# Kernel tuning notes

Measured on AMD Instinct MI355X. Metric: run time of the kernel, lower is better.

Reference implementation:

```python
import jax, jax.numpy as jnp
import numpy as np

DT = 0.05
DELAY = int(1.0 / DT)  # 20 steps of synaptic delay
NUM_ASCS = 2
R_MEM = 0.1     # membrane resistance
SIGMA_V = 1.0   # sigmoid smoothing of spiking nonlinearity
V_RESET = 0.0

B, T, IN, HID, OUT = 64, 200, 512, 1024, 512


def setup_inputs() -> dict:
    key = jax.random.key(0)
    ks = jax.random.split(key, 10)
    return {
        "x": jax.random.normal(ks[0], (B, T, IN), dtype=jnp.float32),
        "W_in": jax.random.normal(ks[1], (IN, HID), dtype=jnp.float32) / np.sqrt(IN),
        "W_lat": jax.random.normal(ks[2], (HID, HID), dtype=jnp.float32) / np.sqrt(HID),
        "thresh": jax.random.normal(ks[3], (1, HID), dtype=jnp.float32) * 0.1,
        "trans_k_m": jax.random.normal(ks[4], (1, HID), dtype=jnp.float32) * 0.1,
        "trans_asc_k": jax.random.normal(ks[5], (NUM_ASCS, 1, HID), dtype=jnp.float32) * 0.1,
        "asc_amp": jax.random.normal(ks[6], (NUM_ASCS, 1, HID), dtype=jnp.float32) * 0.1,
        "trans_asc_r": jax.random.normal(ks[7], (NUM_ASCS, 1, HID), dtype=jnp.float32) * 0.1,
        "W_out": jax.random.normal(ks[8], (OUT, HID), dtype=jnp.float32) / np.sqrt(HID),
        "b_out": jax.random.normal(ks[9], (OUT,), dtype=jnp.float32) * 0.01,
    }


def _glifr_rnn(x, W_in, W_lat, thresh, trans_k_m, trans_asc_k, asc_amp, trans_asc_r, W_out, b_out):
    Bx, Tx, _ = x.shape
    H = W_lat.shape[0]
    # rate transforms keep dt*k in (0,1); r in (-1,1)
    k_m = jax.nn.sigmoid(trans_k_m) / DT          # [1,H]
    k_asc = jax.nn.sigmoid(trans_asc_k) / DT      # [A,1,H]
    asc_r = 1.0 - 2.0 * jax.nn.sigmoid(trans_asc_r)
    # precompute input projection for all timesteps: [T,B,H]
    x_proj = jnp.swapaxes(jnp.einsum("bti,ih->bth", x, W_in), 0, 1)

    def step(carry, xp):
        firing, voltage, asc, buf = carry
        firing_delayed = buf[0]                       # firing DELAY steps ago
        syn = xp + firing_delayed @ W_lat             # synaptic current [B,H]
        asc_new = (asc_amp + asc_r * asc) * firing * (DT * k_asc) + (1.0 - DT * k_asc) * asc
        volt_new = (R_MEM * DT * k_m) * (syn + asc_new.sum(0)) \
                   + (1.0 - DT * k_m) * voltage + DT * k_m * V_RESET
        firing_new = jax.nn.sigmoid((volt_new - thresh) / SIGMA_V)
        buf_new = jnp.concatenate([buf[1:], firing_new[None]], axis=0)
        out = firing_new @ W_out.T + b_out            # per-step linear readout
        return (firing_new, volt_new, asc_new, buf_new), out

    z = jnp.zeros((Bx, H), dtype=x.dtype)
    carry0 = (z, z, jnp.zeros((NUM_ASCS, Bx, H), x.dtype), jnp.zeros((DELAY, Bx, H), x.dtype))
    _, outs = jax.lax.scan(step, carry0, x_proj)      # outs: [T,B,OUT]
    return jnp.swapaxes(outs, 0, 1)                   # [B,T,OUT]


def reference(x, W_in, W_lat, thresh, trans_k_m, trans_asc_k, asc_amp, trans_asc_r, W_out, b_out):
    return _glifr_rnn(x, W_in, W_lat, thresh, trans_k_m, trans_asc_k, asc_amp, trans_asc_r, W_out, b_out)
```

## Files before the change

kernel.cpp:

```cpp
#include <hip/hip_runtime.h>


typedef float f32x4 __attribute__((ext_vector_type(4)));
typedef __bf16 bf16x8 __attribute__((ext_vector_type(8)));
typedef unsigned short ushortx8 __attribute__((ext_vector_type(8)));
typedef unsigned short ushortx4 __attribute__((ext_vector_type(4)));

__device__ __forceinline__ unsigned short f2b(float f) {
    unsigned int u = __float_as_uint(f);
    unsigned int r = u + 0x7FFFu + ((u >> 16) & 1u);
    return (unsigned short)(r >> 16);
}
__device__ __forceinline__ float sigmoidf(float x) {
    return 1.0f / (1.0f + __expf(-x));
}

__device__ __forceinline__ void gl_lds16(const unsigned short* g, unsigned short* l) {
    __builtin_amdgcn_global_load_lds(
        (const __attribute__((address_space(1))) void*)g,
        (__attribute__((address_space(3))) void*)l, 16, 0, 0);
}

__global__ __launch_bounds__(256) void prep_all(
    const float* __restrict__ W_in, const float* __restrict__ W_lat,
    const float* __restrict__ W_out, const float* __restrict__ x,
    unsigned short* __restrict__ WinT, unsigned short* __restrict__ WlatT,
    unsigned short* __restrict__ WoutB, unsigned short* __restrict__ xb)
{
    __shared__ unsigned short t[64][65];
    const int blk = blockIdx.x, tid = threadIdx.x;

    if (blk < 128) {
        int bx = (blk & 15) * 64, by = (blk >> 4) * 64;
        int tx = tid & 63, ty = tid >> 6;
        for (int r = ty; r < 64; r += 4)
            t[r][tx] = f2b(W_in[(size_t)(by + r) * 1024 + bx + tx]);
        __syncthreads();
        for (int r = ty; r < 64; r += 4)
            WinT[(size_t)(bx + r) * 512 + by + tx] = t[tx][r];
    } else if (blk < 384) {
        int b2 = blk - 128;
        int bx = (b2 & 15) * 64, by = (b2 >> 4) * 64;
        int tx = tid & 63, ty = tid >> 6;
        for (int r = ty; r < 64; r += 4)
            t[r][tx] = f2b(W_lat[(size_t)(by + r) * 1024 + bx + tx]);
        __syncthreads();
        for (int r = ty; r < 64; r += 4)
            WlatT[(size_t)(bx + r) * 1024 + by + tx] = t[tx][r];
    } else if (blk < 896) {
        int i = ((blk - 384) * 256 + tid) * 4;
        f32x4 v = *(const f32x4*)(W_out + i);
        ushortx4 o;
        o[0] = f2b(v[0]); o[1] = f2b(v[1]); o[2] = f2b(v[2]); o[3] = f2b(v[3]);
        *(ushortx4*)(WoutB + i) = o;
    } else {
        size_t i8 = (size_t)((blk - 896) * 256 + tid) * 8;
        int m = (int)(i8 >> 9), k = (int)(i8 & 511);
        int b = m & 63, tt = m >> 6;
        const float* src = x + ((size_t)b * 200 + tt) * 512 + k;
        f32x4 v0 = *(const f32x4*)src;
        f32x4 v1 = *(const f32x4*)(src + 4);
        ushortx8 o;
        o[0] = f2b(v0[0]); o[1] = f2b(v0[1]); o[2] = f2b(v0[2]); o[3] = f2b(v0[3]);
        o[4] = f2b(v1[0]); o[5] = f2b(v1[1]); o[6] = f2b(v1[2]); o[7] = f2b(v1[3]);
        *(ushortx8*)(xb + i8) = o;
    }
}

template<int BM, int BN, int MODE>
__global__ __launch_bounds__(256) void gemm_nt(
    const unsigned short* __restrict__ A,
    const unsigned short* __restrict__ Bt,
    float* __restrict__ outf,
    const float* __restrict__ bias,
    int M, int N, int K, int t_base)
{
    constexpr int WM = BM / 2, WN = BN / 2;
    constexpr int TM = WM / 16, TN = WN / 16;

    __shared__ unsigned short Asm[BM * 64];
    __shared__ unsigned short Bsm[BN * 64];

    const int tid  = threadIdx.x;
    const int wave = tid >> 6, lane = tid & 63;
    const int m16  = lane & 15, quad = lane >> 4;
    const int bm0  = blockIdx.y * BM, bn0 = blockIdx.x * BN;
    const int wr   = (wave >> 1) * WM, wc = (wave & 1) * WN;
    const int sr   = lane >> 3;
    const int sc   = lane & 7;

    f32x4 acc[TM][TN];
#pragma unroll
    for (int i = 0; i < TM; i++)
#pragma unroll
        for (int j = 0; j < TN; j++)
            acc[i][j] = (f32x4){0.f, 0.f, 0.f, 0.f};

    for (int k0 = 0; k0 < K; k0 += 64) {
#pragma unroll
        for (int g = wave; g < BM / 8; g += 4) {
            int r = g * 8 + sr;
            int c = sc ^ (r & 7);
            gl_lds16(A + (size_t)(bm0 + r) * K + k0 + c * 8, Asm + g * 512);
        }
#pragma unroll
        for (int g = wave; g < BN / 8; g += 4) {
            int r = g * 8 + sr;
            int c = sc ^ (r & 7);
            gl_lds16(Bt + (size_t)(bn0 + r) * K + k0 + c * 8, Bsm + g * 512);
        }
        __syncthreads();

        ushortx8 af[2][TM], bfr[2][TN];
#pragma unroll
        for (int kh = 0; kh < 2; kh++) {
#pragma unroll
            for (int i = 0; i < TM; i++) {
                int ra = wr + i * 16 + m16;
                af[kh][i] = *(const ushortx8*)(
                    Asm + ra * 64 + (((kh * 4 + quad) ^ (ra & 7)) * 8));
            }
#pragma unroll
            for (int j = 0; j < TN; j++) {
                int rb = wc + j * 16 + m16;
                bfr[kh][j] = *(const ushortx8*)(
                    Bsm + rb * 64 + (((kh * 4 + quad) ^ (rb & 7)) * 8));
            }
        }
#pragma unroll
        for (int i = 0; i < TM; i++)
#pragma unroll
            for (int j = 0; j < TN; j++) {
                acc[i][j] = __builtin_amdgcn_mfma_f32_16x16x32_bf16(
                    __builtin_bit_cast(bf16x8, af[0][i]),
                    __builtin_bit_cast(bf16x8, bfr[0][j]),
                    acc[i][j], 0, 0, 0);
                acc[i][j] = __builtin_amdgcn_mfma_f32_16x16x32_bf16(
                    __builtin_bit_cast(bf16x8, af[1][i]),
                    __builtin_bit_cast(bf16x8, bfr[1][j]),
                    acc[i][j], 0, 0, 0);
            }
        __syncthreads();
    }

#pragma unroll
    for (int i = 0; i < TM; i++)
#pragma unroll
        for (int j = 0; j < TN; j++) {
            int col = bn0 + wc + j * 16 + m16;
            float bv = (MODE == 2) ? bias[col] : 0.f;
#pragma unroll
            for (int v = 0; v < 4; v++) {
                int row = bm0 + wr + i * 16 + quad * 4 + v;
                if (MODE == 2) {
                    size_t o = (size_t)((row & 63) * 200 + t_base + (row >> 6)) * N + col;
                    outf[o] = acc[i][j][v] + bv;
                } else {
                    outf[(size_t)row * N + col] = acc[i][j][v];
                }
            }
        }
}

__global__ __launch_bounds__(256) void fused_chunk(
    const unsigned short* __restrict__ Fprev,
    const unsigned short* __restrict__ Wlat,
    const float* __restrict__ xproj,
    float* __restrict__ state,
    unsigned short* __restrict__ Fc,
    const float* __restrict__ thresh,
    const float* __restrict__ t_km,
    const float* __restrict__ t_ak,
    const float* __restrict__ amp,
    const float* __restrict__ t_ar)
{
    const int BH = 64 * 1024;
    __shared__ __align__(16) char lds[147456];
    unsigned short* A0 = (unsigned short*)lds;
    unsigned short* A1 = (unsigned short*)(lds + 40960);
    unsigned short* B0 = (unsigned short*)(lds + 81920);
    unsigned short* B1 = (unsigned short*)(lds + 114688);
    float* synT = (float*)lds;

    const int tid  = threadIdx.x;
    const int wave = tid >> 6, lane = tid & 63;
    const int m16  = lane & 15, quad = lane >> 4;
    const int sr2  = lane >> 5;
    const int sc32 = lane & 31;
    const int b0   = blockIdx.y * 4, h0 = blockIdx.x * 64;
    const int wrow = (wave >> 1) * 48;
    const int wc   = (wave & 1) * 32;

    f32x4 acc[3][2];
#pragma unroll
    for (int i = 0; i < 3; i++) {
        if (i < 2 || wave < 2) {
#pragma unroll
            for (int j = 0; j < 2; j++)
#pragma unroll
                for (int v = 0; v < 4; v++) {
                    int row = wrow + i * 16 + quad * 4 + v;
                    int col = h0 + wc + j * 16 + m16;
                    acc[i][j][v] = xproj[(size_t)(((row >> 2) << 6) + b0 + (row & 3)) * 1024 + col];
                }
        }
    }

    auto STAGE = [&](unsigned short* Ad, unsigned short* Bd, int k0) {
        for (int g = wave; g < 40; g += 4) {
            int r = g * 2 + sr2;
            int c = sc32 ^ (r & 31);
            int m = ((r >> 2) << 6) + b0 + (r & 3);
            gl_lds16(Fprev + (size_t)m * 1024 + k0 + c * 8, Ad + g * 512);
        }
        for (int g = wave; g < 32; g += 4) {
            int r = g * 2 + sr2;
            int c = sc32 ^ (r & 31);
            gl_lds16(Wlat + (size_t)(h0 + r) * 1024 + k0 + c * 8, Bd + g * 512);
        }
    };
    auto COMPUTE = [&](const unsigned short* As, const unsigned short* Bs) {
#pragma unroll
        for (int half = 0; half < 2; half++) {
            ushortx8 af[4][3], bfr[4][2];
#pragma unroll
            for (int kh = 0; kh < 4; kh++) {
                int s = half * 16 + kh * 4 + quad;
#pragma unroll
                for (int i = 0; i < 3; i++) {
                    if (i < 2 || wave < 2) {
                        int ra = wrow + i * 16 + m16;
                        af[kh][i] = *(const ushortx8*)(
                            As + ra * 256 + ((s ^ (ra & 31)) * 8));
                    }
                }
#pragma unroll
                for (int j = 0; j < 2; j++) {
                    int rb = wc + j * 16 + m16;
                    bfr[kh][j] = *(const ushortx8*)(
                        Bs + rb * 256 + ((s ^ (rb & 31)) * 8));
                }
            }
#pragma unroll
            for (int i = 0; i < 3; i++) {
                if (i < 2 || wave < 2) {
#pragma unroll
                    for (int j = 0; j < 2; j++) {
#pragma unroll
                        for (int kh = 0; kh < 4; kh++) {
                            acc[i][j] = __builtin_amdgcn_mfma_f32_16x16x32_bf16(
                                __builtin_bit_cast(bf16x8, af[kh][i]),
                                __builtin_bit_cast(bf16x8, bfr[kh][j]), acc[i][j], 0, 0, 0);
                        }
                    }
                }
            }
        }
    };

    STAGE(A0, B0, 0);
    __syncthreads();
    STAGE(A1, B1, 256);  COMPUTE(A0, B0);  __syncthreads();
    STAGE(A0, B0, 512);  COMPUTE(A1, B1);  __syncthreads();
    STAGE(A1, B1, 768);  COMPUTE(A0, B0);  __syncthreads();
                         COMPUTE(A1, B1);  __syncthreads();

#pragma unroll
    for (int i = 0; i < 3; i++) {
        if (i < 2 || wave < 2) {
#pragma unroll
            for (int j = 0; j < 2; j++)
#pragma unroll
                for (int v = 0; v < 4; v++) {
                    int row = wrow + i * 16 + quad * 4 + v;
                    synT[row * 66 + wc + j * 16 + m16] = acc[i][j][v];
                }
        }
    }
    __syncthreads();

    const int h    = h0 + lane;
    const int gidx = (b0 + wave) * 1024 + h;
    float th  = thresh[h];
    float sm  = sigmoidf(t_km[h]);
    float rm  = 0.1f * sm;
    float om  = 1.0f - sm;
    float sa0 = sigmoidf(t_ak[h]);
    float sa1 = sigmoidf(t_ak[1024 + h]);
    float am0 = amp[h];
    float am1 = amp[1024 + h];
    float r0  = 1.0f - 2.0f * sigmoidf(t_ar[h]);
    float r1  = 1.0f - 2.0f * sigmoidf(t_ar[1024 + h]);

    float volt = state[gidx];
    float a0   = state[BH + gidx];
    float a1   = state[2 * BH + gidx];
    float fir  = state[3 * BH + gidx];

#pragma unroll
    for (int s = 0; s < 20; s++) {
        float sv  = synT[(s * 4 + wave) * 66 + lane];
        float na0 = (am0 + r0 * a0) * fir * sa0 + (1.f - sa0) * a0;
        float na1 = (am1 + r1 * a1) * fir * sa1 + (1.f - sa1) * a1;
        volt = rm * (sv + na0 + na1) + om * volt;
        fir  = sigmoidf(volt - th);
        Fc[(size_t)s * BH + gidx] = f2b(fir);
        a0 = na0; a1 = na1;
    }
    state[gidx]          = volt;
    state[BH + gidx]     = a0;
    state[2 * BH + gidx] = a1;
    state[3 * BH + gidx] = fir;
}

__global__ __launch_bounds__(256) void chunk_step(
    const float* __restrict__ syn,
    float* __restrict__ state,
    unsigned short* __restrict__ F,
    const float* __restrict__ thresh,
    const float* __restrict__ t_km,
    const float* __restrict__ t_ak,
    const float* __restrict__ amp,
    const float* __restrict__ t_ar)
{
    const int BH = 64 * 1024;
    int idx = blockIdx.x * 256 + threadIdx.x;
    int h = idx & 1023;

    float th  = thresh[h];
    float sm  = sigmoidf(t_km[h]);
    float rm  = 0.1f * sm;
    float om  = 1.0f - sm;
    float sa0 = sigmoidf(t_ak[h]);
    float sa1 = sigmoidf(t_ak[1024 + h]);
    float am0 = amp[h];
    float am1 = amp[1024 + h];
    float r0  = 1.0f - 2.0f * sigmoidf(t_ar[h]);
    float r1  = 1.0f - 2.0f * sigmoidf(t_ar[1024 + h]);

    float volt = 0.f, a0 = 0.f, a1 = 0.f, fir = 0.f;

#pragma unroll
    for (int s = 0; s < 20; s++) {
        float sv  = syn[(size_t)s * BH + idx];
        float na0 = (am0 + r0 * a0) * fir * sa0 + (1.f - sa0) * a0;
        float na1 = (am1 + r1 * a1) * fir * sa1 + (1.f - sa1) * a1;
        volt = rm * (sv + na0 + na1) + om * volt;
        fir  = sigmoidf(volt - th);
        F[(size_t)s * BH + idx] = f2b(fir);
        a0 = na0; a1 = na1;
    }
    state[idx]          = volt;
    state[BH + idx]     = a0;
    state[2 * BH + idx] = a1;
    state[3 * BH + idx] = fir;
}

extern "C" void kernel_launch(void* const* d_in, const int* in_sizes, int n_in,
                              void* d_out, int out_size, void* d_ws, size_t ws_size,
                              hipStream_t stream)
{
    const float* x      = (const float*)d_in[0];
    const float* W_in   = (const float*)d_in[1];
    const float* W_lat  = (const float*)d_in[2];
    const float* thresh = (const float*)d_in[3];
    const float* t_km   = (const float*)d_in[4];
    const float* t_ak   = (const float*)d_in[5];
    const float* amp    = (const float*)d_in[6];
    const float* t_ar   = (const float*)d_in[7];
    const float* W_out  = (const float*)d_in[8];
    const float* b_out  = (const float*)d_in[9];
    float* out = (float*)d_out;

    char* ws = (char*)d_ws;
    float*          syn   = (float*)ws;
    float*          state = (float*)(ws + 52428800);
    unsigned short* F     = (unsigned short*)(ws + 53477376);
    unsigned short* xb    = F;
    unsigned short* WinT  = (unsigned short*)(ws + 79691776);
    unsigned short* WlatT = (unsigned short*)(ws + 80740352);
    unsigned short* WoutB = (unsigned short*)(ws + 82837504);

    prep_all<<<4096, 256, 0, stream>>>(W_in, W_lat, W_out, x,
                                       WinT, WlatT, WoutB, xb);

    gemm_nt<128, 128, 0><<<dim3(1024 / 128, 12800 / 128), 256, 0, stream>>>(
        xb, WinT, syn, nullptr, 12800, 1024, 512, 0);

    chunk_step<<<256, 256, 0, stream>>>(syn, state, F, thresh, t_km, t_ak, amp, t_ar);

    const size_t CHUNK = 20 * 64 * 1024;
    for (int c = 1; c < 10; c++) {
        fused_chunk<<<dim3(16, 16), 256, 0, stream>>>(
            F + (size_t)(c - 1) * CHUNK, WlatT,
            syn + (size_t)c * CHUNK, state, F + (size_t)c * CHUNK,
            thresh, t_km, t_ak, amp, t_ar);
    }

    gemm_nt<128, 128, 2><<<dim3(512 / 128, 12800 / 128), 256, 0, stream>>>(
        F, WoutB, out, b_out, 12800, 512, 1024, 0);
}
```

Baseline: 252.8 us.

## Fuse input projection GEMM into per-chunk recurrent kernel

```diff
diff --git a/kernel.cpp b/kernel.cpp
--- a/kernel.cpp
+++ b/kernel.cpp
@@ -163,9 +163,10 @@
 }
 
 __global__ __launch_bounds__(256) void fused_chunk(
+    const unsigned short* __restrict__ xbc,
     const unsigned short* __restrict__ Fprev,
+    const unsigned short* __restrict__ WinT,
     const unsigned short* __restrict__ Wlat,
-    const float* __restrict__ xproj,
     float* __restrict__ state,
     unsigned short* __restrict__ Fc,
     const float* __restrict__ thresh,
@@ -193,30 +194,24 @@
 
     f32x4 acc[3][2];
 #pragma unroll
-    for (int i = 0; i < 3; i++) {
-        if (i < 2 || wave < 2) {
-#pragma unroll
-            for (int j = 0; j < 2; j++)
-#pragma unroll
-                for (int v = 0; v < 4; v++) {
-                    int row = wrow + i * 16 + quad * 4 + v;
-                    int col = h0 + wc + j * 16 + m16;
-                    acc[i][j][v] = xproj[(size_t)(((row >> 2) << 6) + b0 + (row & 3)) * 1024 + col];
-                }
-        }
-    }
-
-    auto STAGE = [&](unsigned short* Ad, unsigned short* Bd, int k0) {
+    for (int i = 0; i < 3; i++)
+#pragma unroll
+        for (int j = 0; j < 2; j++)
+            acc[i][j] = (f32x4){0.f, 0.f, 0.f, 0.f};
+
+    auto STAGE = [&](unsigned short* Ad, unsigned short* Bd,
+                     const unsigned short* Ab, int As,
+                     const unsigned short* Bb, int Bs, int k0) {
         for (int g = wave; g < 40; g += 4) {
             int r = g * 2 + sr2;
             int c = sc32 ^ (r & 31);
             int m = ((r >> 2) << 6) + b0 + (r & 3);
-            gl_lds16(Fprev + (size_t)m * 1024 + k0 + c * 8, Ad + g * 512);
+            gl_lds16(Ab + (size_t)m * As + k0 + c * 8, Ad + g * 512);
         }
         for (int g = wave; g < 32; g += 4) {
             int r = g * 2 + sr2;
             int c = sc32 ^ (r & 31);
-            gl_lds16(Wlat + (size_t)(h0 + r) * 1024 + k0 + c * 8, Bd + g * 512);
+            gl_lds16(Bb + (size_t)(h0 + r) * Bs + k0 + c * 8, Bd + g * 512);
         }
     };
     auto COMPUTE = [&](const unsigned short* As, const unsigned short* Bs) {
@@ -258,12 +253,14 @@
         }
     };
 
-    STAGE(A0, B0, 0);
+    STAGE(A0, B0, xbc, 512, WinT, 512, 0);
     __syncthreads();
-    STAGE(A1, B1, 256);  COMPUTE(A0, B0);  __syncthreads();
-    STAGE(A0, B0, 512);  COMPUTE(A1, B1);  __syncthreads();
-    STAGE(A1, B1, 768);  COMPUTE(A0, B0);  __syncthreads();
-                         COMPUTE(A1, B1);  __syncthreads();
+    STAGE(A1, B1, xbc,   512,  WinT, 512,  256);  COMPUTE(A0, B0);  __syncthreads();
+    STAGE(A0, B0, Fprev, 1024, Wlat, 1024, 0);    COMPUTE(A1, B1);  __syncthreads();
+    STAGE(A1, B1, Fprev, 1024, Wlat, 1024, 256);  COMPUTE(A0, B0);  __syncthreads();
+    STAGE(A0, B0, Fprev, 1024, Wlat, 1024, 512);  COMPUTE(A1, B1);  __syncthreads();
+    STAGE(A1, B1, Fprev, 1024, Wlat, 1024, 768);  COMPUTE(A0, B0);  __syncthreads();
+                                                  COMPUTE(A1, B1);  __syncthreads();
 
 #pragma unroll
     for (int i = 0; i < 3; i++) {
@@ -374,26 +371,28 @@
 
     char* ws = (char*)d_ws;
     float*          syn   = (float*)ws;
-    float*          state = (float*)(ws + 52428800);
-    unsigned short* F     = (unsigned short*)(ws + 53477376);
-    unsigned short* xb    = F;
-    unsigned short* WinT  = (unsigned short*)(ws + 79691776);
-    unsigned short* WlatT = (unsigned short*)(ws + 80740352);
-    unsigned short* WoutB = (unsigned short*)(ws + 82837504);
+    unsigned short* xb    = (unsigned short*)(ws + 5242880);
+    float*          state = (float*)(ws + 18350080);
+    unsigned short* F     = (unsigned short*)(ws + 19398656);
+    unsigned short* WinT  = (unsigned short*)(ws + 45613056);
+    unsigned short* WlatT = (unsigned short*)(ws + 46661632);
+    unsigned short* WoutB = (unsigned short*)(ws + 48758784);
 
     prep_all<<<4096, 256, 0, stream>>>(W_in, W_lat, W_out, x,
                                        WinT, WlatT, WoutB, xb);
 
-    gemm_nt<128, 128, 0><<<dim3(1024 / 128, 12800 / 128), 256, 0, stream>>>(
-        xb, WinT, syn, nullptr, 12800, 1024, 512, 0);
+    gemm_nt<128, 128, 0><<<dim3(1024 / 128, 1280 / 128), 256, 0, stream>>>(
+        xb, WinT, syn, nullptr, 1280, 1024, 512, 0);
 
     chunk_step<<<256, 256, 0, stream>>>(syn, state, F, thresh, t_km, t_ak, amp, t_ar);
 
-    const size_t CHUNK = 20 * 64 * 1024;
+    const size_t CHUNK  = 20 * 64 * 1024;
+    const size_t CHUNKX = 20 * 64 * 512;
     for (int c = 1; c < 10; c++) {
         fused_chunk<<<dim3(16, 16), 256, 0, stream>>>(
-            F + (size_t)(c - 1) * CHUNK, WlatT,
-            syn + (size_t)c * CHUNK, state, F + (size_t)c * CHUNK,
+            xb + (size_t)c * CHUNKX,
+            F + (size_t)(c - 1) * CHUNK,
+            WinT, WlatT, state, F + (size_t)c * CHUNK,
             thresh, t_km, t_ak, amp, t_ar);
     }
 
```

Measured after the change: 255.6 us. About the same (+1.1%).
